# Optimization experiments

Measured on AMD Instinct MI355X. Metric: run time of the kernel, lower is better.

## Reference

```python
import jax, jax.numpy as jnp
import numpy as np

D_X, D_K, D_V = 1024, 128, 128
B, N = 8, 2048


def setup_inputs() -> dict:
    key = jax.random.key(0)
    ks = jax.random.split(key, 7)
    s = lambda fan_in: 1.0 / np.sqrt(fan_in)
    return {
        "x": jax.random.normal(ks[0], (B, N, D_X), dtype=jnp.float32),
        "w_q": jax.random.uniform(ks[1], (D_K, D_X), jnp.float32, -s(D_X), s(D_X)),
        "b_q": jax.random.uniform(ks[2], (D_K,), jnp.float32, -s(D_X), s(D_X)),
        "w_k": jax.random.uniform(ks[3], (D_K, D_X), jnp.float32, -s(D_X), s(D_X)),
        "b_k": jax.random.uniform(ks[4], (D_K,), jnp.float32, -s(D_X), s(D_X)),
        "w_v": jax.random.uniform(ks[5], (D_V, D_X), jnp.float32, -s(D_X), s(D_X)),
        "b_v": jax.random.uniform(ks[6], (D_V,), jnp.float32, -s(D_X), s(D_X)),
    }


def reference(x, w_q, b_q, w_k, b_k, w_v, b_v):
    # Q is computed in the original module but unused; omit (no effect on output).
    K = jnp.einsum('bnx,kx->bnk', x, w_k) + b_k  # [B,N,d_k]
    V = jnp.einsum('bnx,vx->bnv', x, w_v) + b_v  # [B,N,d_v]
    # logits = K @ V^T / sqrt(d_k)  -> [B,N,N]  (note: K vs V, not Q vs K)
    scale = 1.0 / np.sqrt(D_K).astype(np.float32)
    logits = jnp.einsum('bnk,bmk->bnm', K, V) * scale
    attn = jax.nn.softmax(logits, axis=-1)
    return jnp.einsum('bnm,bmv->bnv', attn, V)
```

## Files before the change

kernel.cpp:

```cpp
#include <hip/hip_runtime.h>
#include <hip/hip_bf16.h>


typedef short s16x8 __attribute__((ext_vector_type(8)));
typedef float f32x4 __attribute__((ext_vector_type(4)));
typedef unsigned short u16;

#define AS1 __attribute__((address_space(1)))
#define AS3 __attribute__((address_space(3)))

__device__ __forceinline__ void gld_lds16(const void* g, void* l) {
  __builtin_amdgcn_global_load_lds((const AS1 unsigned int*)g, (AS3 unsigned int*)l, 16, 0, 0);
}

__device__ __forceinline__ float bf2f(u16 u) {
  unsigned int v = ((unsigned int)u) << 16;
  return __builtin_bit_cast(float, v);
}
__device__ __forceinline__ u16 f2bf(float f) {
  unsigned int u = __builtin_bit_cast(unsigned int, f);
  u += 0x7fffu + ((u >> 16) & 1u);
  return (u16)(u >> 16);
}
__device__ __forceinline__ unsigned pack_bf2(float a, float b) {
  unsigned ua = __builtin_bit_cast(unsigned, a) + 0x8000u;
  unsigned ub = __builtin_bit_cast(unsigned, b) + 0x8000u;
  return __builtin_amdgcn_perm(ub, ua, 0x07060302u);
}

__global__ __launch_bounds__(256, 4) void wconv_kernel(
    const float* __restrict__ wk, const float* __restrict__ wv,
    u16* __restrict__ wbf)
{
  const int e = (blockIdx.x * 256 + threadIdx.x) * 8;
  const float* src = (e < 131072) ? (wk + e) : (wv + (e - 131072));
  float4 a = *(const float4*)src;
  float4 b = *(const float4*)(src + 4);
  union { unsigned u[4]; s16x8 v; } pk;
  pk.u[0] = pack_bf2(a.x, a.y); pk.u[1] = pack_bf2(a.z, a.w);
  pk.u[2] = pack_bf2(b.x, b.y); pk.u[3] = pack_bf2(b.z, b.w);
  *(s16x8*)(wbf + e) = pk.v;
}

__global__ __launch_bounds__(512, 2) void kv_gemm_kernel(
    const float* __restrict__ x, const u16* __restrict__ wbf,
    const float* __restrict__ bk, const float* __restrict__ bv,
    u16* __restrict__ Kout, u16* __restrict__ Vout, u16* __restrict__ VTout)
{
  __shared__ u16 sA[2][8 * 512];
  __shared__ u16 sB[4][32 * 512];

  const int tid  = threadIdx.x;
  const int wave = tid >> 6;
  const int lane = tid & 63;
  const int l16  = lane & 15;
  const int lq   = lane >> 4;
  const int row0 = blockIdx.x * 64;
  const int wr   = wave >> 2;
  const int wc   = wave & 3;

  f32x4 acc[2][4];
  for (int i = 0; i < 2; ++i)
    for (int j = 0; j < 4; ++j) acc[i][j] = (f32x4){0.f, 0.f, 0.f, 0.f};

  const int kc = tid & 7, arow = tid >> 3;
  const float* aSrc = x + (size_t)(row0 + arow) * 1024 + kc * 8;
  const int aSlot = (((arow >> 4) * 2 + (kc >> 2)) * 512) + ((kc & 3) * 16 + (arow & 15)) * 8;

  const u16* bSrc[4];
  for (int i = 0; i < 4; ++i) {
    const int sl = wave + i * 8;
    bSrc[i] = wbf + (size_t)((sl >> 1) * 16 + l16) * 1024 + (sl & 1) * 32 + lq * 8;
  }

  for (int i = 0; i < 4; ++i)
    gld_lds16(bSrc[i], &sB[0][(wave + i * 8) * 512]);
  float4 p0a = *(const float4*)(aSrc);
  float4 p0b = *(const float4*)(aSrc + 4);
  for (int i = 0; i < 4; ++i)
    gld_lds16(bSrc[i] + 64, &sB[1][(wave + i * 8) * 512]);
  float4 p1a = *(const float4*)(aSrc + 64);
  float4 p1b = *(const float4*)(aSrc + 68);

#pragma unroll
  for (int s = 0; s < 16; ++s) {
    const int buf2 = s & 1, buf4 = s & 3;
    {
      union { unsigned u[4]; s16x8 v; } pk;
      pk.u[0] = pack_bf2(p0a.x, p0a.y); pk.u[1] = pack_bf2(p0a.z, p0a.w);
      pk.u[2] = pack_bf2(p0b.x, p0b.y); pk.u[3] = pack_bf2(p0b.z, p0b.w);
      *(s16x8*)(&sA[buf2][aSlot]) = pk.v;
    }
    asm volatile("s_waitcnt lgkmcnt(0)" ::: "memory");
    __builtin_amdgcn_s_barrier();
    if (s == 15) asm volatile("s_waitcnt vmcnt(0)" ::: "memory");
    else         asm volatile("s_waitcnt vmcnt(6)" ::: "memory");
    __builtin_amdgcn_sched_barrier(0);

    if (s + 2 < 16) {
      for (int i = 0; i < 4; ++i)
        gld_lds16(bSrc[i] + (s + 2) * 64, &sB[(s + 2) & 3][(wave + i * 8) * 512]);
    }
    p0a = p1a; p0b = p1b;
    if (s + 2 < 16) {
      p1a = *(const float4*)(aSrc + (s + 2) * 64);
      p1b = *(const float4*)(aSrc + (s + 2) * 64 + 4);
    }

    s16x8 af[2][2], bfr[4][2];
    for (int rb = 0; rb < 2; ++rb)
      for (int ks = 0; ks < 2; ++ks)
        af[rb][ks] = *(const s16x8*)(&sA[buf2][(((wr * 2 + rb) * 2 + ks) * 64 + lane) * 8]);
    for (int cb = 0; cb < 4; ++cb)
      for (int ks = 0; ks < 2; ++ks)
        bfr[cb][ks] = *(const s16x8*)(&sB[buf4][(((wc * 4 + cb) * 2 + ks) * 64 + lane) * 8]);
    for (int rb = 0; rb < 2; ++rb)
      for (int cb = 0; cb < 4; ++cb)
        for (int ks = 0; ks < 2; ++ks)
          acc[rb][cb] = __builtin_amdgcn_mfma_f32_16x16x32_bf16(af[rb][ks], bfr[cb][ks], acc[rb][cb], 0, 0, 0);
  }

  const int  colBase = wc * 64;
  const bool isV = (wc >= 2);
  u16* outN = isV ? Vout : Kout;
  float fbias[4];
  for (int cb = 0; cb < 4; ++cb) {
    const int col = colBase + cb * 16 + l16;
    fbias[cb] = isV ? bv[col - 128] : bk[col];
  }
  for (int rb = 0; rb < 2; ++rb) {
    const int grow0 = row0 + wr * 32 + rb * 16 + lq * 4;
    for (int cb = 0; cb < 4; ++cb) {
      const int gcol = colBase + cb * 16 + l16;
      const int ocol = isV ? (gcol - 128) : gcol;
      union { u16 u[4]; unsigned long long ull; } pk;
      for (int r = 0; r < 4; ++r) {
        u16 h = f2bf(acc[rb][cb][r] + fbias[cb]);
        outN[(size_t)(grow0 + r) * 128 + ocol] = h;
        pk.u[r] = h;
      }
      if (isV) {
        const int bidx = grow0 >> 11;
        const int n    = grow0 & 2047;
        *(unsigned long long*)(VTout + (size_t)bidx * 128 * 2048 + (size_t)ocol * 2048 + n) = pk.ull;
      }
    }
  }
}

__global__ __launch_bounds__(256, 2) void flash_kernel(
    const u16* __restrict__ Kmat, const u16* __restrict__ Vmat,
    const u16* __restrict__ VT, float* __restrict__ out,
    float* __restrict__ Opart, float* __restrict__ lbuf)
{
  __shared__ u16 sV[2][16 * 512];
  __shared__ u16 sVT[2][16 * 512];
  __shared__ u16 sP[64 * 66];

  const int tid  = threadIdx.x;
  const int wave = tid >> 6;
  const int lane = tid & 63;
  const int l16  = lane & 15;
  const int lq   = lane >> 4;
  const int b    = blockIdx.y;
  const int q0   = blockIdx.x * 64;
  const int z    = blockIdx.z;
  const int ntiles = (2048 / gridDim.z) / 64;
  const int mstart = z * (2048 / gridDim.z);
  const float scale = 0.08838834764831845f;

  s16x8 kf[4];
  {
    const u16* Kb = Kmat + ((size_t)b * 2048 + q0 + wave * 16 + l16) * 128 + lq * 8;
    for (int ks = 0; ks < 4; ++ks) kf[ks] = *(const s16x8*)(Kb + ks * 32);
  }

  const u16* vSrc[4];  const u16* vtSrc[4];
  {
    const u16* Vb  = Vmat + (size_t)b * 2048 * 128;
    const u16* VTb = VT   + (size_t)b * 128 * 2048;
    for (int i = 0; i < 4; ++i) {
      const int sl = wave + i * 4;
      vSrc[i]  = Vb  + (size_t)((sl >> 2) * 16 + l16) * 128 + (sl & 3) * 32 + lq * 8;
      vtSrc[i] = VTb + (size_t)((sl >> 1) * 16 + l16) * 2048 + (sl & 1) * 32 + lq * 8;
    }
  }

  f32x4 oacc[8];
  for (int v = 0; v < 8; ++v) oacc[v] = (f32x4){0.f, 0.f, 0.f, 0.f};
  float lrow[4] = {0.f, 0.f, 0.f, 0.f};

  for (int i = 0; i < 4; ++i) {
    gld_lds16(vSrc[i] + (size_t)mstart * 128, &sV[0][(wave + i * 4) * 512]);
    gld_lds16(vtSrc[i] + mstart,              &sVT[0][(wave + i * 4) * 512]);
  }

  for (int mt = 0; mt < ntiles; ++mt) {
    const int buf = mt & 1;
    __syncthreads();
    if (mt + 1 < ntiles) {
      const int m1 = mstart + (mt + 1) * 64;
      for (int i = 0; i < 4; ++i) {
        gld_lds16(vSrc[i] + (size_t)m1 * 128, &sV[buf ^ 1][(wave + i * 4) * 512]);
        gld_lds16(vtSrc[i] + m1,              &sVT[buf ^ 1][(wave + i * 4) * 512]);
      }
    }

    f32x4 sacc[4];
    for (int t = 0; t < 4; ++t) sacc[t] = (f32x4){0.f, 0.f, 0.f, 0.f};
    for (int ks = 0; ks < 4; ++ks)
      for (int t = 0; t < 4; ++t)
        sacc[t] = __builtin_amdgcn_mfma_f32_16x16x32_bf16(
            kf[ks], *(const s16x8*)(&sV[buf][(t * 4 + ks) * 512 + lane * 8]), sacc[t], 0, 0, 0);

    for (int r = 0; r < 4; ++r) {
      const int prow = (wave * 16 + lq * 4 + r) * 66;
      float rs = 0.f;
      for (int t = 0; t < 4; ++t) {
        float p = __expf(sacc[t][r] * scale);
        u16 h = f2bf(p);
        sP[prow + t * 16 + l16] = h;
        rs += bf2f(h);
      }
      lrow[r] += rs;
    }

    for (int ksm = 0; ksm < 2; ++ksm) {
      s16x8 a = *(const s16x8*)(&sP[(wave * 16 + l16) * 66 + ksm * 32 + lq * 8]);
      for (int v = 0; v < 8; ++v)
        oacc[v] = __builtin_amdgcn_mfma_f32_16x16x32_bf16(
            a, *(const s16x8*)(&sVT[buf][(v * 2 + ksm) * 512 + lane * 8]), oacc[v], 0, 0, 0);
    }
  }

  for (int r = 0; r < 4; ++r) {
    lrow[r] += __shfl_xor(lrow[r], 1);
    lrow[r] += __shfl_xor(lrow[r], 2);
    lrow[r] += __shfl_xor(lrow[r], 4);
    lrow[r] += __shfl_xor(lrow[r], 8);
  }

  const size_t rowg = (size_t)b * 2048 + q0 + wave * 16;
  if (gridDim.z == 1) {
    for (int r = 0; r < 4; ++r) {
      const float inv = 1.f / lrow[r];
      for (int v = 0; v < 8; ++v)
        out[(rowg + lq * 4 + r) * 128 + v * 16 + l16] = oacc[v][r] * inv;
    }
  } else {
    float* Op = Opart + (size_t)z * 2097152;
    float* lp = lbuf + (size_t)z * 32768;
    for (int r = 0; r < 4; ++r)
      for (int v = 0; v < 8; ++v)
        Op[(rowg + lq * 4 + r) * 128 + v * 16 + l16] = oacc[v][r];
    if (l16 == 0)
      for (int r = 0; r < 4; ++r)
        lp[rowg + lq * 4 + r] = lrow[r];
  }
}

__global__ __launch_bounds__(256, 4) void combine_kernel(
    const float* __restrict__ Opart, const float* __restrict__ lbuf,
    float* __restrict__ out)
{
  const int idx = blockIdx.x * 256 + threadIdx.x;
  const int row = idx >> 5;
  const float4 o0 = ((const float4*)Opart)[idx];
  const float4 o1 = ((const float4*)(Opart + 2097152))[idx];
  const float inv = 1.f / (lbuf[row] + lbuf[32768 + row]);
  float4 o;
  o.x = (o0.x + o1.x) * inv;
  o.y = (o0.y + o1.y) * inv;
  o.z = (o0.z + o1.z) * inv;
  o.w = (o0.w + o1.w) * inv;
  ((float4*)out)[idx] = o;
}

extern "C" void kernel_launch(void* const* d_in, const int* in_sizes, int n_in,
                              void* d_out, int out_size, void* d_ws, size_t ws_size,
                              hipStream_t stream) {
  const float* x  = (const float*)d_in[0];
  const float* wk = (const float*)d_in[3];
  const float* bk = (const float*)d_in[4];
  const float* wv = (const float*)d_in[5];
  const float* bv = (const float*)d_in[6];

  u16* ws   = (u16*)d_ws;
  u16* wbf  = ws;
  u16* Kmat = ws + 262144;
  u16* Vmat = Kmat + (size_t)16384 * 128;
  u16* VTm  = Vmat + (size_t)16384 * 128;
  float* Opart = (float*)(VTm + (size_t)16384 * 128);
  float* lbuf  = Opart + 2 * 2097152;
  const bool split = ws_size >= (size_t)30200000;

  wconv_kernel<<<128, 256, 0, stream>>>(wk, wv, wbf);
  kv_gemm_kernel<<<256, 512, 0, stream>>>(x, wbf, bk, bv, Kmat, Vmat, VTm);
  if (split) {
    flash_kernel<<<dim3(32, 8, 2), 256, 0, stream>>>(Kmat, Vmat, VTm,
                                                     (float*)d_out, Opart, lbuf);
    combine_kernel<<<2048, 256, 0, stream>>>(Opart, lbuf, (float*)d_out);
  } else {
    flash_kernel<<<dim3(32, 8, 1), 256, 0, stream>>>(Kmat, Vmat, VTm,
                                                     (float*)d_out, Opart, lbuf);
  }
}
```

Before: 170.9 us.

## Process two 16-row query blocks per wave to reuse V fragments and swizzle P

Each wave now handles 32 query rows (two 16-row blocks), so every V and V^T fragment loaded from LDS feeds two MFMAs, and the grid shrinks to 128 rows per block. The P scratch buffer changes from padded rows to an XOR-swizzled 64-wide layout to avoid bank conflicts. Launch bounds drop to one block per CU because accumulator registers double. This cuts LDS read traffic per MFMA but halves the block count and the waves available to hide latency.

After: 180.7 us. +5.7%, slower.

```diff
diff --git a/kernel.cpp b/kernel.cpp
--- a/kernel.cpp
+++ b/kernel.cpp
@@ -148,14 +148,14 @@
   }
 }
 
-__global__ __launch_bounds__(256, 2) void flash_kernel(
+__global__ __launch_bounds__(256, 1) void flash_kernel(
     const u16* __restrict__ Kmat, const u16* __restrict__ Vmat,
     const u16* __restrict__ VT, float* __restrict__ out,
     float* __restrict__ Opart, float* __restrict__ lbuf)
 {
   __shared__ u16 sV[2][16 * 512];
   __shared__ u16 sVT[2][16 * 512];
-  __shared__ u16 sP[64 * 66];
+  __shared__ u16 sP[128 * 64];
 
   const int tid  = threadIdx.x;
   const int wave = tid >> 6;
@@ -163,16 +163,18 @@
   const int l16  = lane & 15;
   const int lq   = lane >> 4;
   const int b    = blockIdx.y;
-  const int q0   = blockIdx.x * 64;
+  const int q0   = blockIdx.x * 128;
   const int z    = blockIdx.z;
   const int ntiles = (2048 / gridDim.z) / 64;
   const int mstart = z * (2048 / gridDim.z);
   const float scale = 0.08838834764831845f;
 
-  s16x8 kf[4];
+  s16x8 kf[2][4];
   {
-    const u16* Kb = Kmat + ((size_t)b * 2048 + q0 + wave * 16 + l16) * 128 + lq * 8;
-    for (int ks = 0; ks < 4; ++ks) kf[ks] = *(const s16x8*)(Kb + ks * 32);
+    const u16* Kb = Kmat + ((size_t)b * 2048 + q0 + wave * 32 + l16) * 128 + lq * 8;
+    for (int rb = 0; rb < 2; ++rb)
+      for (int ks = 0; ks < 4; ++ks)
+        kf[rb][ks] = *(const s16x8*)(Kb + rb * 2048 + ks * 32);
   }
 
   const u16* vSrc[4];  const u16* vtSrc[4];
@@ -186,9 +188,10 @@
     }
   }
 
-  f32x4 oacc[8];
-  for (int v = 0; v < 8; ++v) oacc[v] = (f32x4){0.f, 0.f, 0.f, 0.f};
-  float lrow[4] = {0.f, 0.f, 0.f, 0.f};
+  f32x4 oacc[2][8];
+  for (int rb = 0; rb < 2; ++rb)
+    for (int v = 0; v < 8; ++v) oacc[rb][v] = (f32x4){0.f, 0.f, 0.f, 0.f};
+  float lrow[2][4] = {{0.f, 0.f, 0.f, 0.f}, {0.f, 0.f, 0.f, 0.f}};
 
   for (int i = 0; i < 4; ++i) {
     gld_lds16(vSrc[i] + (size_t)mstart * 128, &sV[0][(wave + i * 4) * 512]);
@@ -206,56 +209,71 @@
       }
     }
 
-    f32x4 sacc[4];
-    for (int t = 0; t < 4; ++t) sacc[t] = (f32x4){0.f, 0.f, 0.f, 0.f};
-    for (int ks = 0; ks < 4; ++ks)
-      for (int t = 0; t < 4; ++t)
-        sacc[t] = __builtin_amdgcn_mfma_f32_16x16x32_bf16(
-            kf[ks], *(const s16x8*)(&sV[buf][(t * 4 + ks) * 512 + lane * 8]), sacc[t], 0, 0, 0);
-
+    f32x4 sacc[2][4];
+    for (int rb = 0; rb < 2; ++rb)
+      for (int t = 0; t < 4; ++t) sacc[rb][t] = (f32x4){0.f, 0.f, 0.f, 0.f};
+    for (int t = 0; t < 4; ++t)
+      for (int ks = 0; ks < 4; ++ks) {
+        const s16x8 bv = *(const s16x8*)(&sV[buf][(t * 4 + ks) * 512 + lane * 8]);
+        sacc[0][t] = __builtin_amdgcn_mfma_f32_16x16x32_bf16(kf[0][ks], bv, sacc[0][t], 0, 0, 0);
+        sacc[1][t] = __builtin_amdgcn_mfma_f32_16x16x32_bf16(kf[1][ks], bv, sacc[1][t], 0, 0, 0);
+      }
+
+    for (int rb = 0; rb < 2; ++rb)
+      for (int r = 0; r < 4; ++r) {
+        const int row = wave * 32 + rb * 16 + lq * 4 + r;
+        const int xr  = (row & 7) << 3;
+        float rs = 0.f;
+        for (int t = 0; t < 4; ++t) {
+          float p = __expf(sacc[rb][t][r] * scale);
+          u16 h = f2bf(p);
+          sP[row * 64 + ((t * 16 + l16) ^ xr)] = h;
+          rs += bf2f(h);
+        }
+        lrow[rb][r] += rs;
+      }
+
+    for (int ksm = 0; ksm < 2; ++ksm) {
+      s16x8 a[2];
+      for (int rb = 0; rb < 2; ++rb) {
+        const int row = wave * 32 + rb * 16 + l16;
+        a[rb] = *(const s16x8*)(&sP[row * 64 + ((ksm * 32 + lq * 8) ^ ((row & 7) << 3))]);
+      }
+      for (int v = 0; v < 8; ++v) {
+        const s16x8 bvt = *(const s16x8*)(&sVT[buf][(v * 2 + ksm) * 512 + lane * 8]);
+        oacc[0][v] = __builtin_amdgcn_mfma_f32_16x16x32_bf16(a[0], bvt, oacc[0][v], 0, 0, 0);
+        oacc[1][v] = __builtin_amdgcn_mfma_f32_16x16x32_bf16(a[1], bvt, oacc[1][v], 0, 0, 0);
+      }
+    }
+  }
+
+  for (int rb = 0; rb < 2; ++rb)
     for (int r = 0; r < 4; ++r) {
-      const int prow = (wave * 16 + lq * 4 + r) * 66;
-      float rs = 0.f;
-      for (int t = 0; t < 4; ++t) {
-        float p = __expf(sacc[t][r] * scale);
-        u16 h = f2bf(p);
-        sP[prow + t * 16 + l16] = h;
-        rs += bf2f(h);
-      }
-      lrow[r] += rs;
-    }
-
-    for (int ksm = 0; ksm < 2; ++ksm) {
-      s16x8 a = *(const s16x8*)(&sP[(wave * 16 + l16) * 66 + ksm * 32 + lq * 8]);
-      for (int v = 0; v < 8; ++v)
-        oacc[v] = __builtin_amdgcn_mfma_f32_16x16x32_bf16(
-            a, *(const s16x8*)(&sVT[buf][(v * 2 + ksm) * 512 + lane * 8]), oacc[v], 0, 0, 0);
-    }
-  }
-
-  for (int r = 0; r < 4; ++r) {
-    lrow[r] += __shfl_xor(lrow[r], 1);
-    lrow[r] += __shfl_xor(lrow[r], 2);
-    lrow[r] += __shfl_xor(lrow[r], 4);
-    lrow[r] += __shfl_xor(lrow[r], 8);
-  }
-
-  const size_t rowg = (size_t)b * 2048 + q0 + wave * 16;
+      lrow[rb][r] += __shfl_xor(lrow[rb][r], 1);
+      lrow[rb][r] += __shfl_xor(lrow[rb][r], 2);
+      lrow[rb][r] += __shfl_xor(lrow[rb][r], 4);
+      lrow[rb][r] += __shfl_xor(lrow[rb][r], 8);
+    }
+
+  const size_t rowg0 = (size_t)b * 2048 + q0 + wave * 32;
   if (gridDim.z == 1) {
-    for (int r = 0; r < 4; ++r) {
-      const float inv = 1.f / lrow[r];
-      for (int v = 0; v < 8; ++v)
-        out[(rowg + lq * 4 + r) * 128 + v * 16 + l16] = oacc[v][r] * inv;
-    }
+    for (int rb = 0; rb < 2; ++rb)
+      for (int r = 0; r < 4; ++r) {
+        const float inv = 1.f / lrow[rb][r];
+        for (int v = 0; v < 8; ++v)
+          out[(rowg0 + rb * 16 + lq * 4 + r) * 128 + v * 16 + l16] = oacc[rb][v][r] * inv;
+      }
   } else {
     float* Op = Opart + (size_t)z * 2097152;
     float* lp = lbuf + (size_t)z * 32768;
-    for (int r = 0; r < 4; ++r)
-      for (int v = 0; v < 8; ++v)
-        Op[(rowg + lq * 4 + r) * 128 + v * 16 + l16] = oacc[v][r];
+    for (int rb = 0; rb < 2; ++rb)
+      for (int r = 0; r < 4; ++r)
+        for (int v = 0; v < 8; ++v)
+          Op[(rowg0 + rb * 16 + lq * 4 + r) * 128 + v * 16 + l16] = oacc[rb][v][r];
     if (l16 == 0)
-      for (int r = 0; r < 4; ++r)
-        lp[rowg + lq * 4 + r] = lrow[r];
+      for (int rb = 0; rb < 2; ++rb)
+        for (int r = 0; r < 4; ++r)
+          lp[rowg0 + rb * 16 + lq * 4 + r] = lrow[rb][r];
   }
 }
 
@@ -297,11 +315,11 @@
   wconv_kernel<<<128, 256, 0, stream>>>(wk, wv, wbf);
   kv_gemm_kernel<<<256, 512, 0, stream>>>(x, wbf, bk, bv, Kmat, Vmat, VTm);
   if (split) {
-    flash_kernel<<<dim3(32, 8, 2), 256, 0, stream>>>(Kmat, Vmat, VTm,
+    flash_kernel<<<dim3(16, 8, 2), 256, 0, stream>>>(Kmat, Vmat, VTm,
                                                      (float*)d_out, Opart, lbuf);
     combine_kernel<<<2048, 256, 0, stream>>>(Opart, lbuf, (float*)d_out);
   } else {
-    flash_kernel<<<dim3(32, 8, 1), 256, 0, stream>>>(Kmat, Vmat, VTm,
+    flash_kernel<<<dim3(16, 8, 1), 256, 0, stream>>>(Kmat, Vmat, VTm,
                                                      (float*)d_out, Opart, lbuf);
   }
 }
```
